# Kernel tuning notes

Hardware: AMD Instinct MI355X
Metric: run time of the kernel (lower is better)

The kernel has to match this reference:

```python
import jax, jax.numpy as jnp
import numpy as np

B, C, H, W = 8, 64, 16, 16
TE = 128      # te_hidden
GT = 256      # rn_gt_hidden
FP = 256      # rn_fp_hidden
A = 32        # a_size
O = H * W
PAIR_IN = (C + 2) * 2 + TE  # 260, matches (cv_filter+2)*2 + te_hidden


def setup_inputs() -> dict:
    key = jax.random.key(0)
    ks = jax.random.split(key, 10)

    def w(k, fan_in, fan_out):
        return (jax.random.normal(k, (fan_in, fan_out), jnp.float32)
                / np.sqrt(fan_in).astype(np.float32))

    return {
        "x": jax.random.normal(ks[0], (B, C, H, W), jnp.float32),
        "code": jax.random.normal(ks[1], (B, TE), jnp.float32),
        "gt_w1": w(ks[2], PAIR_IN, GT), "gt_b1": jnp.zeros((GT,), jnp.float32),
        "gt_w2": w(ks[3], GT, GT),      "gt_b2": jnp.zeros((GT,), jnp.float32),
        "gt_w3": w(ks[4], GT, GT),      "gt_b3": jnp.zeros((GT,), jnp.float32),
        "fp_w1": w(ks[5], GT, FP),      "fp_b1": jnp.zeros((FP,), jnp.float32),
        "fp_w2": w(ks[6], FP, FP),      "fp_b2": jnp.zeros((FP,), jnp.float32),
        "fp_w3": w(ks[7], FP, A),       "fp_b3": jnp.zeros((A,), jnp.float32),
    }


def _coords(h, w):
    # 2 normalized coordinate channels in [-1, 1], one value per object
    ys = jnp.linspace(-1.0, 1.0, h, dtype=jnp.float32)
    xs = jnp.linspace(-1.0, 1.0, w, dtype=jnp.float32)
    yy, xx = jnp.meshgrid(ys, xs, indexing="ij")
    return jnp.stack([yy.ravel(), xx.ravel()], axis=-1)  # (o, 2)


def reference(x, code, gt_w1, gt_b1, gt_w2, gt_b2, gt_w3, gt_b3,
              fp_w1, fp_b1, fp_w2, fp_b2, fp_w3, fp_b3):
    b, c, h, w = x.shape
    o = h * w
    te = code.shape[-1]

    # rn_encode: flatten spatial grid to objects, append 2 coord channels
    xo = x.reshape(b, c, o).transpose(0, 2, 1)                 # (b, o, c)
    coord = jnp.broadcast_to(_coords(h, w)[None], (b, o, 2))
    xo = jnp.concatenate([xo, coord], axis=-1)                 # (b, o, c+2)

    # all O^2 ordered pairs + broadcast question code
    xi = jnp.broadcast_to(xo[:, :, None, :], (b, o, o, c + 2))
    xj = jnp.broadcast_to(xo[:, None, :, :], (b, o, o, c + 2))
    q = jnp.broadcast_to(code[:, None, None, :], (b, o, o, te))
    pairs = jnp.concatenate([xi, xj, q], axis=-1)              # (b, o, o, PAIR_IN)

    # g_theta MLP (ReLU after every layer)
    h1 = jax.nn.relu(pairs @ gt_w1 + gt_b1)
    h2 = jax.nn.relu(h1 @ gt_w2 + gt_b2)
    rel = jax.nn.relu(h2 @ gt_w3 + gt_b3)                      # (b, o, o, GT)

    # lower_sum: sum relations over the lower-triangular (i >= j) pairs
    mask = jnp.tril(jnp.ones((o, o), rel.dtype))
    summed = jnp.einsum("bijd,ij->bd", rel, mask)              # (b, GT)

    # f_phi MLP; no activation on final logits, dropout=0 (eval)
    f1 = jax.nn.relu(summed @ fp_w1 + fp_b1)
    f2 = jax.nn.relu(f1 @ fp_w2 + fp_b2)
    logits = f2 @ fp_w3 + fp_b3                                # (b, A)
    return logits
```

## Files before the change

### kernel.cpp

```cpp
#include <hip/hip_runtime.h>
#include <stdint.h>


#define NPAIR 32896
#define NPT   129

using short8  = __attribute__((ext_vector_type(8))) short;
using float4v = __attribute__((ext_vector_type(4))) float;

__device__ __forceinline__ float asf(unsigned u) {
    union { unsigned u; float f; } c; c.u = u; return c.f;
}
__device__ __forceinline__ unsigned short f2bf(float f) {
    union { float f; unsigned u; } c; c.f = f;
    unsigned u = c.u;
    u += 0x7FFFu + ((u >> 16) & 1u);
    return (unsigned short)(u >> 16);
}
__device__ __forceinline__ unsigned cvtpk(float lo, float hi) {
    unsigned r;
    asm("v_cvt_pk_bf16_f32 %0, %1, %2" : "=v"(r) : "v"(lo), "v"(hi));
    return r;
}
__device__ __forceinline__ void ij_of(int p, int& i, int& j) {
    float s = sqrtf(8.0f * (float)p + 1.0f);
    i = (int)((s - 1.0f) * 0.5f);
    while ((i + 1) * (i + 2) / 2 <= p) ++i;
    while (i * (i + 1) / 2 > p) --i;
    j = p - i * (i + 1) / 2;
}
__device__ __forceinline__ short8 buildA(uint4 uu, uint4 vv) {
    unsigned ua[4] = {uu.x, uu.y, uu.z, uu.w};
    unsigned va[4] = {vv.x, vv.y, vv.z, vv.w};
    union { unsigned u[4]; short8 s; } c;
    #pragma unroll
    for (int q = 0; q < 4; ++q) {
        float lo = asf(ua[q] << 16)         + asf(va[q] << 16);
        float hi = asf(ua[q] & 0xFFFF0000u) + asf(va[q] & 0xFFFF0000u);
        c.u[q] = cvtpk(fmaxf(lo, 0.f), fmaxf(hi, 0.f));
    }
    return c.s;
}

__global__ __launch_bounds__(256) void k_pre(
    const float* __restrict__ x, const float* __restrict__ code,
    const float* __restrict__ w1, const float* __restrict__ b1,
    const float* __restrict__ w2, const float* __restrict__ w3,
    unsigned short* __restrict__ ub, unsigned short* __restrict__ vb,
    unsigned short* __restrict__ w2t, unsigned short* __restrict__ w3t,
    float* __restrict__ summed)
{
    const int tid = threadIdx.x;
    if (blockIdx.x < 32) {
        const int ig = blockIdx.x, b = blockIdx.y, d = tid;
        float q = b1[d];
        const float* cp = code + b * 128;
        #pragma unroll 8
        for (int t = 0; t < 128; ++t) q += cp[t] * w1[(132 + t) * 256 + d];
        float su[8], sv[8];
        #pragma unroll
        for (int k = 0; k < 8; ++k) { su[k] = q; sv[k] = 0.f; }
        const float* xp = x + (b * 64) * 256 + ig * 8;
        for (int c = 0; c < 64; ++c) {
            const float wu = w1[c * 256 + d];
            const float wv = w1[(66 + c) * 256 + d];
            const float* xc = xp + c * 256;
            #pragma unroll
            for (int k = 0; k < 8; ++k) { su[k] += xc[k] * wu; sv[k] += xc[k] * wv; }
        }
        const float wyu = w1[64 * 256 + d],  wxu = w1[65 * 256 + d];
        const float wyv = w1[130 * 256 + d], wxv = w1[131 * 256 + d];
        #pragma unroll
        for (int k = 0; k < 8; ++k) {
            const int i = ig * 8 + k;
            const float yy = (float)(i >> 4) * (2.0f / 15.0f) - 1.0f;
            const float xx = (float)(i & 15) * (2.0f / 15.0f) - 1.0f;
            ub[(b * 256 + i) * 256 + d] = f2bf(su[k] + yy * wyu + xx * wxu);
            vb[(b * 256 + i) * 256 + d] = f2bf(sv[k] + yy * wyv + xx * wxv);
        }
    } else {
        __shared__ float t[64][65];
        const int y = blockIdx.y;
        summed[y * 256 + tid] = 0.f;
        const int tx = tid & 63, ty = tid >> 6;
        for (int jj = 0; jj < 4; ++jj) {
            const int job = y * 4 + jj;
            const float* src = (job & 16) ? w3 : w2;
            unsigned short* dst = (job & 16) ? w3t : w2t;
            const int k0 = ((job >> 2) & 3) * 64, n0 = (job & 3) * 64;
            __syncthreads();
            #pragma unroll
            for (int r = ty; r < 64; r += 4) t[r][tx] = src[(k0 + r) * 256 + n0 + tx];
            __syncthreads();
            #pragma unroll
            for (int r = ty; r < 64; r += 4) dst[(n0 + r) * 256 + k0 + tx] = f2bf(t[tx][r]);
        }
    }
}

__global__ __launch_bounds__(512) void k_fuse(
    const unsigned short* __restrict__ ub, const unsigned short* __restrict__ vb,
    const unsigned short* __restrict__ w2t, const unsigned short* __restrict__ w3t,
    const float* __restrict__ b2, const float* __restrict__ b3,
    float* __restrict__ summed)
{
    extern __shared__ unsigned short lds[];
    const int tid  = threadIdx.x;
    const int pt   = blockIdx.x, b = blockIdx.y;
    const int lane = tid & 63, w = tid >> 6;
    const int lm   = lane & 15, quad = lane >> 4;

    #pragma unroll
    for (int it = 0; it < 16; ++it) {
        const int idx = it * 512 + tid;
        const int n = idx >> 5, c = idx & 31;
        const uint4 d = *(const uint4*)(w2t + n * 256 + c * 8);
        *(uint4*)(&lds[n * 256 + ((c ^ (n & 7)) << 3)]) = d;
    }

    const unsigned short* up[2];
    const unsigned short* vp[2];
    #pragma unroll
    for (int mt = 0; mt < 2; ++mt) {
        const int p0 = pt * 256 + w * 32 + mt * 16 + lm;
        const int p  = p0 < NPAIR ? p0 : NPAIR - 1;
        int i, j; ij_of(p, i, j);
        up[mt] = ub + ((b * 256 + i) * 256) + quad * 8;
        vp[mt] = vb + ((b * 256 + j) * 256) + quad * 8;
    }
    const int wave_valid = (pt * 256 + w * 32) < NPAIR;
    __syncthreads();

    const float4v zero4 = {0.f, 0.f, 0.f, 0.f};

    float4v acc1[2][16];
    #pragma unroll
    for (int mt = 0; mt < 2; ++mt)
        #pragma unroll
        for (int nt = 0; nt < 16; ++nt) acc1[mt][nt] = zero4;
    {
        uint4 cu[2], cv[2];
        #pragma unroll
        for (int mt = 0; mt < 2; ++mt) {
            cu[mt] = *(const uint4*)(up[mt]);
            cv[mt] = *(const uint4*)(vp[mt]);
        }
        for (int ks = 0; ks < 8; ++ks) {
            uint4 nu[2], nv[2];
            if (ks < 7) {
                #pragma unroll
                for (int mt = 0; mt < 2; ++mt) {
                    nu[mt] = *(const uint4*)(up[mt] + (ks + 1) * 32);
                    nv[mt] = *(const uint4*)(vp[mt] + (ks + 1) * 32);
                }
            }
            short8 afr[2];
            #pragma unroll
            for (int mt = 0; mt < 2; ++mt) afr[mt] = buildA(cu[mt], cv[mt]);
            const int coff = ((ks * 4 + quad) ^ (lm & 7)) << 3;
            __builtin_amdgcn_s_setprio(1);
            #pragma unroll
            for (int ng = 0; ng < 4; ++ng) {
                short8 bfr[4];
                #pragma unroll
                for (int q = 0; q < 4; ++q)
                    bfr[q] = *(const short8*)(&lds[((ng * 4 + q) * 16 + lm) * 256 + coff]);
                #pragma unroll
                for (int mt = 0; mt < 2; ++mt)
                    #pragma unroll
                    for (int q = 0; q < 4; ++q)
                        acc1[mt][ng * 4 + q] = __builtin_amdgcn_mfma_f32_16x16x32_bf16(
                            afr[mt], bfr[q], acc1[mt][ng * 4 + q], 0, 0, 0);
            }
            __builtin_amdgcn_s_setprio(0);
            #pragma unroll
            for (int mt = 0; mt < 2; ++mt) { cu[mt] = nu[mt]; cv[mt] = nv[mt]; }
        }
    }
    __syncthreads();

    const float msk = wave_valid ? 1.f : 0.f;
    #pragma unroll
    for (int nt = 0; nt < 16; ++nt) {
        const float bb = b2[nt * 16 + lm];
        const int col = nt * 16 + lm;
        #pragma unroll
        for (int mt = 0; mt < 2; ++mt) {
            const int rbase = w * 32 + mt * 16 + quad * 4;
            const float v0 = fmaxf(acc1[mt][nt][0] + bb, 0.f) * msk;
            const float v1 = fmaxf(acc1[mt][nt][1] + bb, 0.f) * msk;
            const float v2 = fmaxf(acc1[mt][nt][2] + bb, 0.f) * msk;
            const float v3 = fmaxf(acc1[mt][nt][3] + bb, 0.f) * msk;
            const unsigned w01 = cvtpk(v0, v1), w23 = cvtpk(v2, v3);
            const int c0 = col >> 3, c7 = col & 7;
            lds[(rbase + 0) * 256 + (((c0 ^ ((rbase + 0) & 7)) << 3) | c7)] =
                (unsigned short)w01;
            lds[(rbase + 1) * 256 + (((c0 ^ ((rbase + 1) & 7)) << 3) | c7)] =
                (unsigned short)(w01 >> 16);
            lds[(rbase + 2) * 256 + (((c0 ^ ((rbase + 2) & 7)) << 3) | c7)] =
                (unsigned short)w23;
            lds[(rbase + 3) * 256 + (((c0 ^ ((rbase + 3) & 7)) << 3) | c7)] =
                (unsigned short)(w23 >> 16);
        }
    }
    __syncthreads();

    float4v acc2[16][2];
    #pragma unroll
    for (int mt = 0; mt < 16; ++mt)
        #pragma unroll
        for (int nt = 0; nt < 2; ++nt) acc2[mt][nt] = zero4;
    {
        const unsigned short* bb3 = w3t + ((w * 32 + lm) * 256) + quad * 8;
        short8 bcur[2], bnxt[2];
        #pragma unroll
        for (int nt = 0; nt < 2; ++nt) bcur[nt] = *(const short8*)(bb3 + nt * 4096);
        for (int ks = 0; ks < 8; ++ks) {
            if (ks < 7) {
                #pragma unroll
                for (int nt = 0; nt < 2; ++nt)
                    bnxt[nt] = *(const short8*)(bb3 + nt * 4096 + (ks + 1) * 32);
            }
            __builtin_amdgcn_s_setprio(1);
            #pragma unroll
            for (int mt = 0; mt < 16; ++mt) {
                const int row = mt * 16 + lm;
                const short8 a = *(const short8*)(
                    &lds[row * 256 + (((ks * 4 + quad) ^ (row & 7)) << 3)]);
                #pragma unroll
                for (int nt = 0; nt < 2; ++nt)
                    acc2[mt][nt] = __builtin_amdgcn_mfma_f32_16x16x32_bf16(
                        a, bcur[nt], acc2[mt][nt], 0, 0, 0);
            }
            __builtin_amdgcn_s_setprio(0);
            #pragma unroll
            for (int nt = 0; nt < 2; ++nt) bcur[nt] = bnxt[nt];
        }
    }

    #pragma unroll
    for (int nt = 0; nt < 2; ++nt) {
        const int col = w * 32 + nt * 16 + lm;
        const float bb = b3[col];
        float s = 0.f;
        #pragma unroll
        for (int mt = 0; mt < 16; ++mt)
            #pragma unroll
            for (int rg = 0; rg < 4; ++rg)
                s += fmaxf(acc2[mt][nt][rg] + bb, 0.f);
        s += __shfl_xor(s, 16);
        s += __shfl_xor(s, 32);
        if (quad == 0)
            atomicAdd(&summed[b * 256 + col], s);
    }
}

__global__ __launch_bounds__(1024) void k_tail(
    const float* __restrict__ summed,
    const float* __restrict__ fw1, const float* __restrict__ fb1,
    const float* __restrict__ fw2, const float* __restrict__ fb2,
    const float* __restrict__ fw3, const float* __restrict__ fb3,
    float* __restrict__ out)
{
    __shared__ float s0[256], s1[256], red[1024];
    const int b = blockIdx.x, tid = threadIdx.x;
    const int d = tid & 255, kh = tid >> 8;
    if (tid < 256) s0[tid] = summed[b * 256 + tid];
    __syncthreads();
    float p = 0.f;
    #pragma unroll 16
    for (int k = kh * 64; k < kh * 64 + 64; ++k) p += s0[k] * fw1[k * 256 + d];
    red[kh * 256 + d] = p;
    __syncthreads();
    if (tid < 256)
        s1[tid] = fmaxf(red[tid] + red[256 + tid] + red[512 + tid] + red[768 + tid]
                        + fb1[tid], 0.f);
    __syncthreads();
    p = 0.f;
    #pragma unroll 16
    for (int k = kh * 64; k < kh * 64 + 64; ++k) p += s1[k] * fw2[k * 256 + d];
    red[kh * 256 + d] = p;
    __syncthreads();
    if (tid < 256)
        s0[tid] = fmaxf(red[tid] + red[256 + tid] + red[512 + tid] + red[768 + tid]
                        + fb2[tid], 0.f);
    __syncthreads();
    const int d3 = tid & 31, kh3 = tid >> 5;
    p = 0.f;
    #pragma unroll
    for (int k = kh3 * 8; k < kh3 * 8 + 8; ++k) p += s0[k] * fw3[k * 32 + d3];
    red[kh3 * 32 + d3] = p;
    __syncthreads();
    if (tid < 32) {
        float o = fb3[tid];
        #pragma unroll 8
        for (int r = 0; r < 32; ++r) o += red[r * 32 + tid];
        out[b * 32 + tid] = o;
    }
}

extern "C" void kernel_launch(void* const* d_in, const int* in_sizes, int n_in,
                              void* d_out, int out_size, void* d_ws, size_t ws_size,
                              hipStream_t stream) {
    const float* x    = (const float*)d_in[0];
    const float* code = (const float*)d_in[1];
    const float* gw1  = (const float*)d_in[2];
    const float* gb1  = (const float*)d_in[3];
    const float* gw2  = (const float*)d_in[4];
    const float* gb2  = (const float*)d_in[5];
    const float* gw3  = (const float*)d_in[6];
    const float* gb3  = (const float*)d_in[7];
    const float* fw1  = (const float*)d_in[8];
    const float* fb1  = (const float*)d_in[9];
    const float* fw2  = (const float*)d_in[10];
    const float* fb2  = (const float*)d_in[11];
    const float* fw3  = (const float*)d_in[12];
    const float* fb3  = (const float*)d_in[13];
    float* out = (float*)d_out;

    char* ws = (char*)d_ws;
    unsigned short* ub  = (unsigned short*)(ws);
    unsigned short* vb  = (unsigned short*)(ws + 1048576);
    unsigned short* w2t = (unsigned short*)(ws + 2097152);
    unsigned short* w3t = (unsigned short*)(ws + 2228224);
    float* summed = (float*)(ws + 2359296);

    hipLaunchKernelGGL(k_pre, dim3(33, 8), dim3(256), 0, stream,
                       x, code, gw1, gb1, gw2, gw3, ub, vb, w2t, w3t, summed);
    hipLaunchKernelGGL(k_fuse, dim3(NPT, 8), dim3(512), 131072, stream,
                       ub, vb, w2t, w3t, gb2, gb3, summed);
    hipLaunchKernelGGL(k_tail, dim3(8), dim3(1024), 0, stream,
                       summed, fw1, fb1, fw2, fb2, fw3, fb3, out);
}
```

Before: 194.0 us.

## Fuse f_phi tail MLP into k_fuse via last-blocks completion counter

```diff
diff --git a/kernel.cpp b/kernel.cpp
--- a/kernel.cpp
+++ b/kernel.cpp
@@ -4,6 +4,7 @@
 
 #define NPAIR 32896
 #define NPT   129
+#define TOTAL (NPT * 8)
 
 using short8  = __attribute__((ext_vector_type(8))) short;
 using float4v = __attribute__((ext_vector_type(4))) float;
@@ -48,19 +49,20 @@
     const float* __restrict__ w2, const float* __restrict__ w3,
     unsigned short* __restrict__ ub, unsigned short* __restrict__ vb,
     unsigned short* __restrict__ w2t, unsigned short* __restrict__ w3t,
-    float* __restrict__ summed)
+    float* __restrict__ summed, unsigned* __restrict__ cnt)
 {
     const int tid = threadIdx.x;
     if (blockIdx.x < 32) {
         const int ig = blockIdx.x, b = blockIdx.y, d = tid;
         float q = b1[d];
         const float* cp = code + b * 128;
-        #pragma unroll 8
+        #pragma unroll 16
         for (int t = 0; t < 128; ++t) q += cp[t] * w1[(132 + t) * 256 + d];
         float su[8], sv[8];
         #pragma unroll
         for (int k = 0; k < 8; ++k) { su[k] = q; sv[k] = 0.f; }
         const float* xp = x + (b * 64) * 256 + ig * 8;
+        #pragma unroll 8
         for (int c = 0; c < 64; ++c) {
             const float wu = w1[c * 256 + d];
             const float wv = w1[(66 + c) * 256 + d];
@@ -82,6 +84,7 @@
         __shared__ float t[64][65];
         const int y = blockIdx.y;
         summed[y * 256 + tid] = 0.f;
+        if (y == 0 && tid == 0) *cnt = 0u;
         const int tx = tid & 63, ty = tid >> 6;
         for (int jj = 0; jj < 4; ++jj) {
             const int job = y * 4 + jj;
@@ -102,7 +105,11 @@
     const unsigned short* __restrict__ ub, const unsigned short* __restrict__ vb,
     const unsigned short* __restrict__ w2t, const unsigned short* __restrict__ w3t,
     const float* __restrict__ b2, const float* __restrict__ b3,
-    float* __restrict__ summed)
+    float* __restrict__ summed, unsigned* __restrict__ cnt,
+    const float* __restrict__ fw1, const float* __restrict__ fb1,
+    const float* __restrict__ fw2, const float* __restrict__ fb2,
+    const float* __restrict__ fw3, const float* __restrict__ fb3,
+    float* __restrict__ out)
 {
     extern __shared__ unsigned short lds[];
     const int tid  = threadIdx.x;
@@ -253,49 +260,58 @@
         if (quad == 0)
             atomicAdd(&summed[b * 256 + col], s);
     }
-}
-
-__global__ __launch_bounds__(1024) void k_tail(
-    const float* __restrict__ summed,
-    const float* __restrict__ fw1, const float* __restrict__ fb1,
-    const float* __restrict__ fw2, const float* __restrict__ fb2,
-    const float* __restrict__ fw3, const float* __restrict__ fb3,
-    float* __restrict__ out)
-{
-    __shared__ float s0[256], s1[256], red[1024];
-    const int b = blockIdx.x, tid = threadIdx.x;
+
+    volatile int* eflag = (volatile int*)(lds + 4096);
+    __threadfence();
+    __syncthreads();
+    if (tid == 0) {
+        unsigned old = __hip_atomic_fetch_add(cnt, 1u, __ATOMIC_ACQ_REL,
+                                              __HIP_MEMORY_SCOPE_AGENT);
+        *eflag = (old >= TOTAL - 8) ? (int)(TOTAL - 1 - old) : -1;
+    }
+    __syncthreads();
+    const int eb = *eflag;
+    if (eb < 0) return;
+    if (tid == 0) {
+        while (__hip_atomic_load(cnt, __ATOMIC_ACQUIRE,
+                                 __HIP_MEMORY_SCOPE_AGENT) < TOTAL)
+            __builtin_amdgcn_s_sleep(2);
+    }
+    __syncthreads();
+
+    float* fs   = (float*)lds;
+    float* fred = fs + 256;
+    float* fact = fs + 768;
     const int d = tid & 255, kh = tid >> 8;
-    if (tid < 256) s0[tid] = summed[b * 256 + tid];
+    if (kh == 0)
+        fs[d] = __hip_atomic_load(&summed[eb * 256 + d], __ATOMIC_RELAXED,
+                                  __HIP_MEMORY_SCOPE_AGENT);
     __syncthreads();
     float p = 0.f;
     #pragma unroll 16
-    for (int k = kh * 64; k < kh * 64 + 64; ++k) p += s0[k] * fw1[k * 256 + d];
-    red[kh * 256 + d] = p;
-    __syncthreads();
-    if (tid < 256)
-        s1[tid] = fmaxf(red[tid] + red[256 + tid] + red[512 + tid] + red[768 + tid]
-                        + fb1[tid], 0.f);
+    for (int k = kh * 128; k < kh * 128 + 128; ++k) p += fs[k] * fw1[k * 256 + d];
+    fred[kh * 256 + d] = p;
+    __syncthreads();
+    if (kh == 0) fact[d] = fmaxf(fred[d] + fred[256 + d] + fb1[d], 0.f);
     __syncthreads();
     p = 0.f;
     #pragma unroll 16
-    for (int k = kh * 64; k < kh * 64 + 64; ++k) p += s1[k] * fw2[k * 256 + d];
-    red[kh * 256 + d] = p;
-    __syncthreads();
-    if (tid < 256)
-        s0[tid] = fmaxf(red[tid] + red[256 + tid] + red[512 + tid] + red[768 + tid]
-                        + fb2[tid], 0.f);
-    __syncthreads();
-    const int d3 = tid & 31, kh3 = tid >> 5;
+    for (int k = kh * 128; k < kh * 128 + 128; ++k) p += fact[k] * fw2[k * 256 + d];
+    fred[kh * 256 + d] = p;
+    __syncthreads();
+    if (kh == 0) fs[d] = fmaxf(fred[d] + fred[256 + d] + fb2[d], 0.f);
+    __syncthreads();
+    const int d3 = tid & 31, g = tid >> 5;
     p = 0.f;
     #pragma unroll
-    for (int k = kh3 * 8; k < kh3 * 8 + 8; ++k) p += s0[k] * fw3[k * 32 + d3];
-    red[kh3 * 32 + d3] = p;
+    for (int k = g * 16; k < g * 16 + 16; ++k) p += fs[k] * fw3[k * 32 + d3];
+    fred[g * 32 + d3] = p;
     __syncthreads();
     if (tid < 32) {
         float o = fb3[tid];
-        #pragma unroll 8
-        for (int r = 0; r < 32; ++r) o += red[r * 32 + tid];
-        out[b * 32 + tid] = o;
+        #pragma unroll
+        for (int r = 0; r < 16; ++r) o += fred[r * 32 + tid];
+        out[eb * 32 + tid] = o;
     }
 }
 
@@ -324,11 +340,11 @@
     unsigned short* w2t = (unsigned short*)(ws + 2097152);
     unsigned short* w3t = (unsigned short*)(ws + 2228224);
     float* summed = (float*)(ws + 2359296);
+    unsigned* cnt = (unsigned*)(ws + 2367488);
 
     hipLaunchKernelGGL(k_pre, dim3(33, 8), dim3(256), 0, stream,
-                       x, code, gw1, gb1, gw2, gw3, ub, vb, w2t, w3t, summed);
+                       x, code, gw1, gb1, gw2, gw3, ub, vb, w2t, w3t, summed, cnt);
     hipLaunchKernelGGL(k_fuse, dim3(NPT, 8), dim3(512), 131072, stream,
-                       ub, vb, w2t, w3t, gb2, gb3, summed);
-    hipLaunchKernelGGL(k_tail, dim3(8), dim3(1024), 0, stream,
-                       summed, fw1, fb1, fw2, fb2, fw3, fb3, out);
-}
+                       ub, vb, w2t, w3t, gb2, gb3, summed, cnt,
+                       fw1, fb1, fw2, fb2, fw3, fb3, out);
+}
```

Measured after the change: 321.5 us. 1.66x slower.
